# Performance work log

Hardware: AMD Instinct MI355X
Metric: run time of the kernel (lower is better)

The kernel has to match this reference:

```python
import jax, jax.numpy as jnp
import numpy as np

B, N, M = 64, 256, 16
ONF, OEF = 92, 41
NF, EF = 128, 64
FINAL = 128  # final_node_len; final_layer outputs FINAL//2


def _linear_params(key, fan_in, fan_out):
    # kaiming_uniform fan_in, relu: bound = sqrt(6/fan_in)
    bound = np.sqrt(6.0 / fan_in)
    W = jax.random.uniform(key, (fan_out, fan_in), jnp.float32, -bound, bound)
    b = jnp.zeros((fan_out,), jnp.float32)
    return W, b


def setup_inputs() -> dict:
    key = jax.random.key(0)
    ks = jax.random.split(key, 12)
    node_fea = jax.random.normal(ks[0], (B, N, ONF), jnp.float32)
    edge_fea = jax.random.normal(ks[1], (B, N, M, OEF), jnp.float32)
    edge_fea_idx = jax.random.randint(ks[2], (B, N, M), 0, N)
    dis = jax.random.uniform(ks[3], (N, N), jnp.float32)
    Wn, bn = _linear_params(ks[4], ONF, NF)
    We, be = _linear_params(ks[5], OEF, EF)
    W1, b1 = _linear_params(ks[6], 2 * NF + EF, 2 * NF)
    W2, b2 = _linear_params(ks[7], 2 * NF + EF, 2 * NF)
    W3, b3 = _linear_params(ks[8], 2 * NF + EF, 2 * NF)
    Wf, bf = _linear_params(ks[9], NF, FINAL // 2)
    return dict(node_fea=node_fea, edge_fea=edge_fea, edge_fea_idx=edge_fea_idx,
                dis=dis, Wn=Wn, bn=bn, We=We, be=be,
                W1=W1, b1=b1, a1=jnp.float32(0.7),
                W2=W2, b2=b2, a2=jnp.float32(0.7),
                W3=W3, b3=b3, a3=jnp.float32(0.7),
                Wf=Wf, bf=bf,
                DAw=jnp.float32(48.0 / 5.0), DAb=jnp.float32(-28.0 / 5.0))


def _conv(nf, ef, idx, W, b, alpha):
    # nf: [B,N,F]; ef: [B,N,M,E]; idx: [B,N,M]
    Bb, Nn, Mm = idx.shape
    F = nf.shape[-1]
    idx_c = jnp.maximum(idx, 0)
    gathered = jax.vmap(lambda x, i: x[i])(nf, idx_c)           # [B,N,M,F]
    self_exp = jnp.broadcast_to(nf[:, :, None, :], (Bb, Nn, Mm, F))
    total = jnp.concatenate([self_exp, gathered, ef], axis=-1)   # [B,N,M,2F+E]
    gated = jnp.einsum('bnmi,oi->bnmo', total, W) + b            # [B,N,M,2F]
    nbr_filter, nbr_core = jnp.split(gated, 2, axis=-1)
    mask = (idx >= 0).astype(nf.dtype)[..., None]
    nbr_filter = jax.nn.sigmoid(nbr_filter) * mask
    nbr_core = jax.nn.softplus(nbr_core)
    nbr_sumed = jnp.sum(nbr_filter * nbr_core, axis=2)           # [B,N,F]
    return jax.nn.softplus(alpha * nf + nbr_sumed)


def reference(node_fea, edge_fea, edge_fea_idx, dis,
              Wn, bn, We, be,
              W1, b1, a1, W2, b2, a2, W3, b3, a3,
              Wf, bf, DAw, DAb):
    nf = node_fea @ Wn.T + bn                                    # [B,N,NF]
    ef = edge_fea @ We.T + be                                    # [B,N,M,EF]
    nf = _conv(nf, ef, edge_fea_idx, W1, b1, a1)
    nf = _conv(nf, ef, edge_fea_idx, W2, b2, a2)
    nf = _conv(nf, ef, edge_fea_idx, W3, b3, a3)
    nf = nf @ Wf.T + bf                                          # [B,N,FINAL//2]
    DA = jax.nn.sigmoid(DAw * dis + DAb)                         # [N,N]
    node1 = jnp.einsum('ij,bjf->bif', DA, nf)
    return jnp.concatenate([nf, node1], axis=2)                  # [B,N,FINAL]
```

## Files before the change

kernel.cpp:

```cpp
#include <hip/hip_runtime.h>
#include <hip/hip_bf16.h>
#include <math.h>

#define Bb   64
#define Nn   256
#define Mm   16
#define ONF  92
#define OEF  41
#define NF   128
#define EF   64
#define KDIM 320
#define ODIM 256
#define FINAL 128
#define K0C  6
#define NGRP  (Bb * Nn / 4)
#define GRIDP 768

#define LOG2E_F 1.44269504088896f
#define LN2_F   0.6931471805599453f

typedef __attribute__((ext_vector_type(8))) short short8;
typedef __attribute__((ext_vector_type(4))) float f32x4;

#define AS1 __attribute__((address_space(1)))
#define AS3 __attribute__((address_space(3)))

__device__ __forceinline__ void gl2lds16(const void* gp, void* lp) {
    __builtin_amdgcn_global_load_lds((AS1 void*)(void*)gp, (AS3 void*)lp, 16, 0, 0);
}
#define KEEP8(x) asm volatile("" : "+v"(x))

__device__ __forceinline__ float sigmoidf_(float x) {
    float e = __expf(-x);
    return __builtin_amdgcn_rcpf(1.0f + e);
}
__device__ __forceinline__ float softplusf_(float x) {
    return fmaxf(x, 0.0f) + __logf(1.0f + __expf(-fabsf(x)));
}
__device__ __forceinline__ __hip_bfloat16 to_bf16(float x) { return __float2bfloat16(x); }

__device__ __forceinline__ void swz(const float* __restrict__ in, __hip_bfloat16* __restrict__ out,
                                    int t, int Itot, int koff, int Kuse, int K0, float scale)
{
    int j = t & 7;
    int u = t >> 3;
    int lane = u & 63;
    int ln16 = lane & 15, q = lane >> 4;
    int v = u >> 6;
    int k0 = v % K0, tile = v / K0;
    int n = tile * 16 + ln16, k = k0 * 32 + q * 8 + j;
    out[t] = (k < Kuse) ? to_bf16(scale * in[(size_t)n * Itot + koff + k]) : to_bf16(0.0f);
}

#define SZ_WET (OEF * EF)
#define SZ_WB  (16 * K0C * 512)
#define SZ_WS  (16 * 4 * 512)
#define SZ_WNB ((NF / 16) * 3 * 512)
#define SZ_WEB ((EF / 16) * 2 * 512)
#define SZ_WFB ((64 / 16) * 4 * 512)
#define SZ_DA  (Nn * Nn)
#define PREP_TOTAL (SZ_WET + 3 * SZ_WB + 3 * SZ_WS + SZ_WNB + SZ_WEB + SZ_WFB + SZ_DA)

__global__ __launch_bounds__(256) void k_prep(
    const float* __restrict__ We, const float* __restrict__ W1,
    const float* __restrict__ W2, const float* __restrict__ W3,
    const float* __restrict__ Wn, const float* __restrict__ Wf,
    const float* __restrict__ dis, const float* __restrict__ pw, const float* __restrict__ pb,
    float* __restrict__ WeT,
    __hip_bfloat16* __restrict__ W1b, __hip_bfloat16* __restrict__ W2b, __hip_bfloat16* __restrict__ W3b,
    __hip_bfloat16* __restrict__ W1s, __hip_bfloat16* __restrict__ W2s, __hip_bfloat16* __restrict__ W3s,
    __hip_bfloat16* __restrict__ Wnb, __hip_bfloat16* __restrict__ Web, __hip_bfloat16* __restrict__ Wfb,
    __hip_bfloat16* __restrict__ DAf)
{
    int t = blockIdx.x * 256 + threadIdx.x;
    if (t < SZ_WET) {
        int o = t / OEF, i = t - o * OEF;
        WeT[i * EF + o] = We[t];
        return;
    }
    t -= SZ_WET;
    if (t < SZ_WB) { swz(W1, W1b, t, KDIM, NF, 192, K0C, LOG2E_F); return; }
    t -= SZ_WB;
    if (t < SZ_WB) { swz(W2, W2b, t, KDIM, NF, 192, K0C, LOG2E_F); return; }
    t -= SZ_WB;
    if (t < SZ_WB) { swz(W3, W3b, t, KDIM, NF, 192, K0C, LOG2E_F); return; }
    t -= SZ_WB;
    if (t < SZ_WS) { swz(W1, W1s, t, KDIM, 0, NF, 4, LOG2E_F); return; }
    t -= SZ_WS;
    if (t < SZ_WS) { swz(W2, W2s, t, KDIM, 0, NF, 4, LOG2E_F); return; }
    t -= SZ_WS;
    if (t < SZ_WS) { swz(W3, W3s, t, KDIM, 0, NF, 4, LOG2E_F); return; }
    t -= SZ_WS;
    if (t < SZ_WNB) { swz(Wn, Wnb, t, ONF, 0, ONF, 3, 1.0f); return; }
    t -= SZ_WNB;
    if (t < SZ_WEB) { swz(We, Web, t, OEF, 0, OEF, 2, 1.0f); return; }
    t -= SZ_WEB;
    if (t < SZ_WFB) { swz(Wf, Wfb, t, NF, 0, NF, 4, 1.0f); return; }
    t -= SZ_WFB;
    if (t < SZ_DA) {
        int i = t >> 8, jx = t & 255;
        float v = sigmoidf_(fmaf(*pw, dis[t], *pb));
        int itile = i >> 4, ln16 = i & 15;
        int k0 = jx >> 5, q = (jx >> 3) & 3, jj = jx & 7;
        DAf[(size_t)((((itile * 8 + k0) << 6) + (q << 4) + ln16)) * 8 + jj] = to_bf16(v);
    }
}

template<int KIN, int K0, int NCOLS>
__device__ __forceinline__ void emb_body(
    int bid, const float* __restrict__ X, const __hip_bfloat16* __restrict__ Bswz,
    const float* __restrict__ bias, __hip_bfloat16* __restrict__ Y,
    __hip_bfloat16* A_s, __hip_bfloat16* O_s)
{
    constexpr int KP = K0 * 32;
    constexpr int TPW = NCOLS / 64;
    constexpr int OLD = NCOLS + 24;

    const int row0 = bid * 64;
    const int t = threadIdx.x;

    {
        const float4* Xb = (const float4*)(X + (size_t)row0 * KIN);
        constexpr int NV = (64 * KIN) / 4;
        for (int c = t; c < NV; c += 256) {
            float4 v = Xb[c];
            int flat = c * 4;
            #pragma unroll
            for (int e = 0; e < 4; e++) {
                int f = flat + e;
                int row = f / KIN, k = f - row * KIN;
                int mt = row >> 4, ln16 = row & 15;
                int k0 = k >> 5, q = (k >> 3) & 3, j = k & 7;
                float vv = (e == 0) ? v.x : (e == 1) ? v.y : (e == 2) ? v.z : v.w;
                A_s[(((mt * K0 + k0) << 6) + (q << 4) + ln16) * 8 + j] = to_bf16(vv);
            }
        }
        constexpr int PAD = KP - KIN;
        for (int c = t; c < 64 * PAD; c += 256) {
            int row = c / PAD, k = KIN + (c - row * PAD);
            int mt = row >> 4, ln16 = row & 15;
            int k0 = k >> 5, q = (k >> 3) & 3, j = k & 7;
            A_s[(((mt * K0 + k0) << 6) + (q << 4) + ln16) * 8 + j] = to_bf16(0.0f);
        }
    }
    __syncthreads();

    const int wv = t >> 6, lane = t & 63;
    const int q = lane >> 4, ln16 = lane & 15;

    f32x4 acc[4][TPW];
    #pragma unroll
    for (int p = 0; p < TPW; p++) {
        float bv = bias[(wv * TPW + p) * 16 + ln16];
        #pragma unroll
        for (int mt = 0; mt < 4; mt++) acc[mt][p] = (f32x4){bv, bv, bv, bv};
    }

    short8 bw[TPW][K0];
    #pragma unroll
    for (int p = 0; p < TPW; p++)
        #pragma unroll
        for (int k0 = 0; k0 < K0; k0++)
            bw[p][k0] = *(const short8*)(Bswz + ((size_t)((wv * TPW + p) * K0 + k0) << 9) + (lane << 3));

    #pragma unroll
    for (int k0 = 0; k0 < K0; k0++) {
        short8 af[4];
        #pragma unroll
        for (int mt = 0; mt < 4; mt++)
            af[mt] = *(const short8*)(A_s + (((mt * K0 + k0) << 6) + lane) * 8);
        #pragma unroll
        for (int mt = 0; mt < 4; mt++)
            #pragma unroll
            for (int p = 0; p < TPW; p++)
                acc[mt][p] = __builtin_amdgcn_mfma_f32_16x16x32_bf16(af[mt], bw[p][k0], acc[mt][p], 0, 0, 0);
    }

    #pragma unroll
    for (int mt = 0; mt < 4; mt++)
        #pragma unroll
        for (int p = 0; p < TPW; p++) {
            int col = (wv * TPW + p) * 16 + ln16;
            #pragma unroll
            for (int r = 0; r < 4; r++)
                O_s[(mt * 16 + q * 4 + r) * OLD + col] = to_bf16(acc[mt][p][r]);
        }
    __syncthreads();
    constexpr int CH = NCOLS / 8;
    for (int c = t; c < 64 * CH; c += 256) {
        int row = c / CH, ch = c - row * CH;
        *(uint4*)(Y + (size_t)(row0 + row) * NCOLS + ch * 8) =
            *(const uint4*)(O_s + row * OLD + ch * 8);
    }
}

__global__ __launch_bounds__(256) void k_embed_all(
    const float* __restrict__ node_fea, const __hip_bfloat16* __restrict__ Wnb,
    const float* __restrict__ bn, __hip_bfloat16* __restrict__ nf0,
    const float* __restrict__ edge_fea, const __hip_bfloat16* __restrict__ Web,
    const float* __restrict__ be, __hip_bfloat16* __restrict__ efb)
{
    __shared__ __align__(16) __hip_bfloat16 A_s[4 * 3 * 512];
    __shared__ __align__(16) __hip_bfloat16 O_s[64 * (NF + 24)];
    if (blockIdx.x < 256)
        emb_body<ONF, 3, NF>(blockIdx.x, node_fea, Wnb, bn, nf0, A_s, O_s);
    else
        emb_body<OEF, 2, EF>(blockIdx.x - 256, edge_fea, Web, be, efb, A_s, O_s);
}

__global__ __launch_bounds__(256) void k_gemm_s(
    const __hip_bfloat16* __restrict__ nf,
    const __hip_bfloat16* __restrict__ Ws,
    const float* __restrict__ bias,
    float* __restrict__ S)
{
    __shared__ __align__(16) __hip_bfloat16 A_s[16 * 512];
    const int row0 = blockIdx.x * 64;
    const int t = threadIdx.x;
    const int wv = t >> 6, lane = t & 63;
    const int q = lane >> 4, ln16 = lane & 15;

    #pragma unroll
    for (int k0 = 0; k0 < 4; k0++)
        gl2lds16(nf + (size_t)(row0 + (wv << 4) + ln16) * NF + k0 * 32 + q * 8,
                 A_s + ((wv * 4 + k0) * 64 + lane) * 8);
    __syncthreads();

    short8 bw[4][4];
    #pragma unroll
    for (int p = 0; p < 4; p++)
        #pragma unroll
        for (int k0 = 0; k0 < 4; k0++)
            bw[p][k0] = *(const short8*)(Ws + ((size_t)((wv * 4 + p) * 4 + k0) << 9) + (lane << 3));

    f32x4 acc[4][4];
    #pragma unroll
    for (int p = 0; p < 4; p++) {
        float bv = bias[(wv * 4 + p) * 16 + ln16] * LOG2E_F;
        #pragma unroll
        for (int mt = 0; mt < 4; mt++) acc[mt][p] = (f32x4){bv, bv, bv, bv};
    }

    #pragma unroll
    for (int k0 = 0; k0 < 4; k0++) {
        short8 af[4];
        #pragma unroll
        for (int mt = 0; mt < 4; mt++)
            af[mt] = *(const short8*)(A_s + ((mt * 4 + k0) * 64 + lane) * 8);
        #pragma unroll
        for (int mt = 0; mt < 4; mt++)
            #pragma unroll
            for (int p = 0; p < 4; p++)
                acc[mt][p] = __builtin_amdgcn_mfma_f32_16x16x32_bf16(af[mt], bw[p][k0], acc[mt][p], 0, 0, 0);
    }

    #pragma unroll
    for (int mt = 0; mt < 4; mt++)
        #pragma unroll
        for (int p = 0; p < 4; p++) {
            int col = (wv * 4 + p) * 16 + ln16;
            #pragma unroll
            for (int r = 0; r < 4; r++)
                S[(size_t)(row0 + mt * 16 + q * 4 + r) * ODIM + col] = acc[mt][p][r];
        }
}

__global__ __launch_bounds__(256, 3) void k_conv_ps(
    const __hip_bfloat16* __restrict__ nf_in,
    const __hip_bfloat16* __restrict__ ef_bf,
    const int*   __restrict__ eidx,
    const __hip_bfloat16* __restrict__ Wb,
    const float* __restrict__ Sbuf,
    const float* __restrict__ palpha,
    __hip_bfloat16* __restrict__ nf_out)
{
    __shared__ __align__(16) __hip_bfloat16 A_s[2][4 * K0C * 512];

    const int t = threadIdx.x;
    const int wv = t >> 6, lane = t & 63;
    const int q = lane >> 4, ln16 = lane & 15;
    const int row = (wv << 4) + ln16;
    const float alpha = *palpha;

    auto stage_group = [&](int gi, __hip_bfloat16* buf) -> unsigned long long {
        const int node0g = gi * 4;
        const int bbase = node0g & ~255;
        int mi = eidx[node0g * Mm + row];
        unsigned long long mb = __ballot(eidx[node0g * Mm + lane] >= 0);
        int j = mi < 0 ? 0 : mi;
        const __hip_bfloat16* gathp = nf_in + (size_t)(bbase + j) * NF + q * 8;
        #pragma unroll
        for (int k0 = 0; k0 < 4; k0++)
            gl2lds16(gathp + k0 * 32, buf + (wv * K0C + k0) * 512 + lane * 8);
        const __hip_bfloat16* efp = ef_bf + (size_t)((node0g << 4) + row) * EF + q * 8;
        #pragma unroll
        for (int k0 = 0; k0 < 2; k0++)
            gl2lds16(efp + k0 * 32, buf + (wv * K0C + 4 + k0) * 512 + lane * 8);
        return mb;
    };

    const __hip_bfloat16* WF0 = Wb + ((size_t)(2 * wv) * (K0C * 512)) + (lane << 3);
    const __hip_bfloat16* WF1 = WF0 + K0C * 512;
    const __hip_bfloat16* WC0 = WF0 + 8 * (K0C * 512);
    const __hip_bfloat16* WC1 = WC0 + K0C * 512;
    short8 mF0[K0C], mF1[K0C], mC0[K0C], mC1[K0C];
    #pragma unroll
    for (int k0 = 0; k0 < K0C; k0++) {
        mF0[k0] = *(const short8*)(WF0 + k0 * 512);
        mF1[k0] = *(const short8*)(WF1 + k0 * 512);
        mC0[k0] = *(const short8*)(WC0 + k0 * 512);
        mC1[k0] = *(const short8*)(WC1 + k0 * 512);
    }

    int g = blockIdx.x;
    unsigned long long mb_pending = stage_group(g, A_s[0]);
    int cur = 0;

    for (; g < NGRP; g += GRIDP) {
        __syncthreads();

        const unsigned long long mb_now = mb_pending;
        if (g + GRIDP < NGRP) mb_pending = stage_group(g + GRIDP, A_s[cur ^ 1]);

        #pragma unroll
        for (int k0 = 0; k0 < K0C; k0++) {
            KEEP8(mF0[k0]); KEEP8(mF1[k0]); KEEP8(mC0[k0]); KEEP8(mC1[k0]);
        }

        const int node0g = g * 4;
        const __hip_bfloat16* Acur = A_s[cur];

        #pragma unroll
        for (int mt = 0; mt < 4; mt++) {
            const int gnode = node0g + mt;
            const float* Srow = Sbuf + (size_t)gnode * ODIM;
            f32x4 accF[2], accC[2];
            float selfv[2];
            #pragma unroll
            for (int p = 0; p < 2; p++) {
                int col = (2 * wv + p) * 16 + ln16;
                float vF = Srow[col];
                float vC = Srow[128 + col];
                accF[p] = (f32x4){vF, vF, vF, vF};
                accC[p] = (f32x4){vC, vC, vC, vC};
                selfv[p] = __bfloat162float(nf_in[(size_t)gnode * NF + col]);
            }
            #pragma unroll
            for (int k0 = 0; k0 < K0C; k0++) {
                short8 af = *(const short8*)(Acur + ((mt * K0C + k0) * 64 + lane) * 8);
                accF[0] = __builtin_amdgcn_mfma_f32_16x16x32_bf16(af, mF0[k0], accF[0], 0, 0, 0);
                accF[1] = __builtin_amdgcn_mfma_f32_16x16x32_bf16(af, mF1[k0], accF[1], 0, 0, 0);
                accC[0] = __builtin_amdgcn_mfma_f32_16x16x32_bf16(af, mC0[k0], accC[0], 0, 0, 0);
                accC[1] = __builtin_amdgcn_mfma_f32_16x16x32_bf16(af, mC1[k0], accC[1], 0, 0, 0);
            }
            unsigned mbits = (unsigned)(mb_now >> (mt * 16 + q * 4)) & 0xFu;
            #pragma unroll
            for (int p = 0; p < 2; p++) {
                float partial = 0.0f;
                #pragma unroll
                for (int r = 0; r < 4; r++) {
                    bool msk = (mbits >> r) & 1u;
                    float f2 = accF[p][r];
                    float c2 = accC[p][r];
                    float sig = __builtin_amdgcn_rcpf(1.0f + __builtin_amdgcn_exp2f(-f2));
                    float sp2 = fmaxf(c2, 0.0f) +
                                __builtin_amdgcn_logf(1.0f + __builtin_amdgcn_exp2f(-fabsf(c2)));
                    partial += msk ? sig * sp2 : 0.0f;
                }
                partial += __shfl_xor(partial, 16);
                partial += __shfl_xor(partial, 32);
                if (q == 0) {
                    int col = (2 * wv + p) * 16 + ln16;
                    nf_out[(size_t)gnode * NF + col] =
                        to_bf16(softplusf_(fmaf(alpha, selfv[p], LN2_F * partial)));
                }
            }
        }
        cur ^= 1;
    }
}

template<bool PRECOMP>
__global__ __launch_bounds__(256, 3) void k_conv_mfma(
    const __hip_bfloat16* __restrict__ nf_in,
    const float* __restrict__ edge_fea,
    const __hip_bfloat16* __restrict__ ef_bf,
    const int*   __restrict__ eidx,
    const float* __restrict__ WeT,
    const float* __restrict__ be,
    const __hip_bfloat16* __restrict__ Wb,
    const __hip_bfloat16* __restrict__ Wsb,
    const float* __restrict__ bias,
    const float* __restrict__ palpha,
    __hip_bfloat16* __restrict__ nf_out)
{
    __shared__ __align__(16) __hip_bfloat16 A_s[4 * K0C * 512];
    __shared__ __align__(16) __hip_bfloat16 A_sf[4 * 512];

    const int node0 = blockIdx.x * 4;
    const int b = node0 >> 8;
    const int t = threadIdx.x;
    const int wv = t >> 6, lane = t & 63;
    const int q = lane >> 4, ln16 = lane & 15;
    const int row = (wv << 4) + ln16;

    const int myidx = eidx[node0 * Mm + row];
    const unsigned long long mball = __ballot(eidx[node0 * Mm + lane] >= 0);

    float selfv[8];
    #pragma unroll
    for (int mt = 0; mt < 4; mt++)
        #pragma unroll
        for (int p = 0; p < 2; p++)
            selfv[mt * 2 + p] =
                __bfloat162float(nf_in[(size_t)(node0 + mt) * NF + (2 * wv + p) * 16 + ln16]);

    {
        int j = myidx < 0 ? 0 : myidx;
        const __hip_bfloat16* gathp = nf_in + (size_t)((b << 8) + j) * NF;
        #pragma unroll
        for (int k0 = 0; k0 < 4; k0++)
            *(uint4*)(A_s + ((wv * K0C + k0) * 64 + lane) * 8) =
                *(const uint4*)(gathp + k0 * 32 + q * 8);
        *(uint4*)(A_sf + (wv * 64 + lane) * 8) =
            *(const uint4*)(nf_in + (size_t)(node0 + (ln16 & 3)) * NF + wv * 32 + q * 8);
        if (PRECOMP) {
            const __hip_bfloat16* efp = ef_bf + (size_t)((node0 << 4) + row) * EF;
            #pragma unroll
            for (int k0 = 0; k0 < 2; k0++)
                *(uint4*)(A_s + ((wv * K0C + 4 + k0) * 64 + lane) * 8) =
                    *(const uint4*)(efp + k0 * 32 + q * 8);
        } else {
            for (int c = t; c < 64 * EF; c += 256) {
                int rr = c >> 6, col = c & 63;
                float a = be[col];
                const float* er = edge_fea + (size_t)(node0 * Mm + rr) * OEF;
                #pragma unroll
                for (int i = 0; i < OEF; i++) a = fmaf(er[i], WeT[i * EF + col], a);
                int mt = rr >> 4, l16 = rr & 15;
                int k0 = 4 + (col >> 5), qq = (col >> 3) & 3, jj = col & 7;
                A_s[((mt * K0C + k0) * 64 + qq * 16 + l16) * 8 + jj] = to_bf16(a);
            }
        }
    }
    __syncthreads();

    f32x4 sv[4];
    #pragma unroll
    for (int c = 0; c < 4; c++) {
        int tile = 2 * wv + (c & 1) + ((c >> 1) << 3);
        float bv = bias[tile * 16 + ln16] * LOG2E_F;
        sv[c] = (f32x4){bv, bv, bv, bv};
    }
    #pragma unroll
    for (int k0 = 0; k0 < 4; k0++) {
        short8 afs = *(const short8*)(A_sf + (k0 * 64 + lane) * 8);
        #pragma unroll
        for (int c = 0; c < 4; c++) {
            int tile = 2 * wv + (c & 1) + ((c >> 1) << 3);
            short8 bws = *(const short8*)(Wsb + ((size_t)(tile * 4 + k0) << 9) + (lane << 3));
            sv[c] = __builtin_amdgcn_mfma_f32_16x16x32_bf16(afs, bws, sv[c], 0, 0, 0);
        }
    }

    f32x4 accF[4][2], accC[4][2];
    #pragma unroll
    for (int mt = 0; mt < 4; mt++) {
        #pragma unroll
        for (int p = 0; p < 2; p++) {
            float vF = __shfl(sv[p][mt], ln16);
            float vC = __shfl(sv[2 + p][mt], ln16);
            accF[mt][p] = (f32x4){vF, vF, vF, vF};
            accC[mt][p] = (f32x4){vC, vC, vC, vC};
        }
    }

    const __hip_bfloat16* WF0 = Wb + ((size_t)(2 * wv) * (K0C * 512)) + (lane << 3);
    const __hip_bfloat16* WF1 = WF0 + K0C * 512;
    const __hip_bfloat16* WC0 = WF0 + 8 * (K0C * 512);
    const __hip_bfloat16* WC1 = WC0 + K0C * 512;

    #pragma unroll
    for (int k0 = 0; k0 < K0C; k0++) {
        short8 cF0 = *(const short8*)(WF0 + k0 * 512);
        short8 cF1 = *(const short8*)(WF1 + k0 * 512);
        short8 cC0 = *(const short8*)(WC0 + k0 * 512);
        short8 cC1 = *(const short8*)(WC1 + k0 * 512);
        short8 af[4];
        #pragma unroll
        for (int mt = 0; mt < 4; mt++)
            af[mt] = *(const short8*)(A_s + ((mt * K0C + k0) * 64 + lane) * 8);
        #pragma unroll
        for (int mt = 0; mt < 4; mt++) {
            accF[mt][0] = __builtin_amdgcn_mfma_f32_16x16x32_bf16(af[mt], cF0, accF[mt][0], 0, 0, 0);
            accF[mt][1] = __builtin_amdgcn_mfma_f32_16x16x32_bf16(af[mt], cF1, accF[mt][1], 0, 0, 0);
            accC[mt][0] = __builtin_amdgcn_mfma_f32_16x16x32_bf16(af[mt], cC0, accC[mt][0], 0, 0, 0);
            accC[mt][1] = __builtin_amdgcn_mfma_f32_16x16x32_bf16(af[mt], cC1, accC[mt][1], 0, 0, 0);
        }
    }

    const float alpha = *palpha;
    #pragma unroll
    for (int mt = 0; mt < 4; mt++) {
        const int gnode = node0 + mt;
        unsigned mbits = (unsigned)(mball >> (mt * 16 + q * 4)) & 0xFu;
        #pragma unroll
        for (int p = 0; p < 2; p++) {
            float partial = 0.0f;
            #pragma unroll
            for (int r = 0; r < 4; r++) {
                bool msk = (mbits >> r) & 1u;
                float f2 = accF[mt][p][r];
                float c2 = accC[mt][p][r];
                float sig = __builtin_amdgcn_rcpf(1.0f + __builtin_amdgcn_exp2f(-f2));
                float sp2 = fmaxf(c2, 0.0f) +
                            __builtin_amdgcn_logf(1.0f + __builtin_amdgcn_exp2f(-fabsf(c2)));
                partial += msk ? sig * sp2 : 0.0f;
            }
            partial += __shfl_xor(partial, 16);
            partial += __shfl_xor(partial, 32);
            if (q == 0) {
                int col = (2 * wv + p) * 16 + ln16;
                nf_out[(size_t)gnode * NF + col] =
                    to_bf16(softplusf_(fmaf(alpha, selfv[mt * 2 + p], LN2_F * partial)));
            }
        }
    }
}

__global__ __launch_bounds__(256) void k_final_mfma(
    const __hip_bfloat16* __restrict__ nf, const __hip_bfloat16* __restrict__ Wfb,
    const float* __restrict__ bfv, float* __restrict__ out,
    __hip_bfloat16* __restrict__ XT)
{
    __shared__ __align__(16) __hip_bfloat16 A_s[16 * 512];
    const int node0 = blockIdx.x * 64;
    const int bloc = node0 >> 8;
    const int t = threadIdx.x;
    const int wv = t >> 6, lane = t & 63;
    const int q = lane >> 4, ln16 = lane & 15;

    const __hip_bfloat16* rowp = nf + (size_t)(node0 + (wv << 4) + ln16) * NF;
    #pragma unroll
    for (int k0 = 0; k0 < 4; k0++)
        *(uint4*)(A_s + ((wv * 4 + k0) * 64 + lane) * 8) =
            *(const uint4*)(rowp + k0 * 32 + q * 8);
    __syncthreads();

    short8 bw[4];
    #pragma unroll
    for (int k0 = 0; k0 < 4; k0++)
        bw[k0] = *(const short8*)(Wfb + ((size_t)(wv * 4 + k0) * 64 + lane) * 8);

    float bv = bfv[wv * 16 + ln16];
    f32x4 acc[4];
    #pragma unroll
    for (int mt = 0; mt < 4; mt++) acc[mt] = (f32x4){bv, bv, bv, bv};

    #pragma unroll
    for (int k0 = 0; k0 < 4; k0++) {
        short8 af[4];
        #pragma unroll
        for (int mt = 0; mt < 4; mt++)
            af[mt] = *(const short8*)(A_s + ((mt * 4 + k0) * 64 + lane) * 8);
        #pragma unroll
        for (int mt = 0; mt < 4; mt++)
            acc[mt] = __builtin_amdgcn_mfma_f32_16x16x32_bf16(af[mt], bw[k0], acc[mt], 0, 0, 0);
    }

    const int col = (wv << 4) + ln16;
    #pragma unroll
    for (int mt = 0; mt < 4; mt++)
        #pragma unroll
        for (int r = 0; r < 4; r++) {
            int row = mt * 16 + q * 4 + r;
            float v = acc[mt][r];
            out[(size_t)(node0 + row) * FINAL + col] = v;
            XT[(size_t)(bloc * 64 + col) * 256 + (node0 & 255) + row] = to_bf16(v);
        }
}

__global__ __launch_bounds__(256) void k_node1_mfma(
    const __hip_bfloat16* __restrict__ DAf,
    const __hip_bfloat16* __restrict__ XT,
    float* __restrict__ out)
{
    __shared__ __align__(16) __hip_bfloat16 B_s[32 * 512];
    const int blk = blockIdx.x;
    const int b = blk >> 2, i0 = (blk & 3) * 64;
    const int t = threadIdx.x;
    const int wv = t >> 6, lane = t & 63;
    const int q = lane >> 4, ln16 = lane & 15;

    const __hip_bfloat16* xrow = XT + (size_t)(b * 64 + (wv << 4) + ln16) * 256;
    #pragma unroll
    for (int k0 = 0; k0 < 8; k0++)
        *(uint4*)(B_s + ((wv * 8 + k0) * 64 + lane) * 8) =
            *(const uint4*)(xrow + k0 * 32 + q * 8);
    __syncthreads();

    f32x4 acc[4];
    #pragma unroll
    for (int mt = 0; mt < 4; mt++) acc[mt] = (f32x4){0.f, 0.f, 0.f, 0.f};

    #pragma unroll
    for (int k0 = 0; k0 < 8; k0++) {
        short8 bfr = *(const short8*)(B_s + ((wv * 8 + k0) * 64 + lane) * 8);
        short8 af[4];
        #pragma unroll
        for (int mt = 0; mt < 4; mt++)
            af[mt] = *(const short8*)(DAf + (size_t)(((i0 >> 4) + mt) * 8 + k0) * 512 + (lane << 3));
        #pragma unroll
        for (int mt = 0; mt < 4; mt++)
            acc[mt] = __builtin_amdgcn_mfma_f32_16x16x32_bf16(af[mt], bfr, acc[mt], 0, 0, 0);
    }

    #pragma unroll
    for (int mt = 0; mt < 4; mt++)
        #pragma unroll
        for (int r = 0; r < 4; r++) {
            int i = i0 + mt * 16 + q * 4 + r;
            out[(size_t)((b << 8) + i) * FINAL + 64 + (wv << 4) + ln16] = acc[mt][r];
        }
}

extern "C" void kernel_launch(void* const* d_in, const int* in_sizes, int n_in,
                              void* d_out, int out_size, void* d_ws, size_t ws_size,
                              hipStream_t stream)
{
    const float* node_fea = (const float*)d_in[0];
    const float* edge_fea = (const float*)d_in[1];
    const int*   eidx     = (const int*)  d_in[2];
    const float* dis      = (const float*)d_in[3];
    const float* Wn = (const float*)d_in[4];
    const float* bn = (const float*)d_in[5];
    const float* We = (const float*)d_in[6];
    const float* be = (const float*)d_in[7];
    const float* W1 = (const float*)d_in[8];
    const float* b1 = (const float*)d_in[9];
    const float* a1 = (const float*)d_in[10];
    const float* W2 = (const float*)d_in[11];
    const float* b2 = (const float*)d_in[12];
    const float* a2 = (const float*)d_in[13];
    const float* W3 = (const float*)d_in[14];
    const float* b3 = (const float*)d_in[15];
    const float* a3 = (const float*)d_in[16];
    const float* Wf = (const float*)d_in[17];
    const float* bf = (const float*)d_in[18];
    const float* DAw = (const float*)d_in[19];
    const float* DAb = (const float*)d_in[20];
    float* out = (float*)d_out;

    char* base = (char*)d_ws;
    size_t off = 0;
    auto alloc = [&](size_t bytes) { char* p = base + off; off = (off + bytes + 255) & ~(size_t)255; return p; };
    __hip_bfloat16* nfA = (__hip_bfloat16*)alloc((size_t)Bb * Nn * NF * 2);
    __hip_bfloat16* nfB = (__hip_bfloat16*)alloc((size_t)Bb * Nn * NF * 2);
    __hip_bfloat16* W1b = (__hip_bfloat16*)alloc((size_t)SZ_WB * 2);
    __hip_bfloat16* W2b = (__hip_bfloat16*)alloc((size_t)SZ_WB * 2);
    __hip_bfloat16* W3b = (__hip_bfloat16*)alloc((size_t)SZ_WB * 2);
    __hip_bfloat16* W1s = (__hip_bfloat16*)alloc((size_t)SZ_WS * 2);
    __hip_bfloat16* W2s = (__hip_bfloat16*)alloc((size_t)SZ_WS * 2);
    __hip_bfloat16* W3s = (__hip_bfloat16*)alloc((size_t)SZ_WS * 2);
    float* WeT = (float*)alloc((size_t)OEF * EF * 4);
    __hip_bfloat16* DAf = (__hip_bfloat16*)alloc((size_t)Nn * Nn * 2);
    __hip_bfloat16* Wnb = (__hip_bfloat16*)alloc((size_t)SZ_WNB * 2);
    __hip_bfloat16* Web = (__hip_bfloat16*)alloc((size_t)SZ_WEB * 2);
    __hip_bfloat16* Wfb = (__hip_bfloat16*)alloc((size_t)SZ_WFB * 2);
    __hip_bfloat16* XT  = (__hip_bfloat16*)alloc((size_t)Bb * 64 * Nn * 2);
    __hip_bfloat16* efb = (__hip_bfloat16*)alloc((size_t)Bb * Nn * Mm * EF * 2);
    float* Sbuf = (float*)alloc((size_t)Bb * Nn * ODIM * 4);
    const bool precomp = (ws_size >= off);

    hipLaunchKernelGGL(k_prep, dim3((PREP_TOTAL + 255) / 256), dim3(256), 0, stream,
                       We, W1, W2, W3, Wn, Wf, dis, DAw, DAb,
                       WeT, W1b, W2b, W3b, W1s, W2s, W3s, Wnb, Web, Wfb, DAf);

    hipLaunchKernelGGL(k_embed_all, dim3(precomp ? (256 + Bb * Nn * Mm / 64) : 256), dim3(256), 0, stream,
                       node_fea, Wnb, bn, nfA, edge_fea, Web, be, efb);

    if (precomp) {
        hipLaunchKernelGGL(k_gemm_s, dim3(Bb * Nn / 64), dim3(256), 0, stream,
                           nfA, W1s, b1, Sbuf);
        hipLaunchKernelGGL(k_conv_ps, dim3(GRIDP), dim3(256), 0, stream,
                           nfA, efb, eidx, W1b, Sbuf, a1, nfB);
        hipLaunchKernelGGL(k_gemm_s, dim3(Bb * Nn / 64), dim3(256), 0, stream,
                           nfB, W2s, b2, Sbuf);
        hipLaunchKernelGGL(k_conv_ps, dim3(GRIDP), dim3(256), 0, stream,
                           nfB, efb, eidx, W2b, Sbuf, a2, nfA);
        hipLaunchKernelGGL(k_gemm_s, dim3(Bb * Nn / 64), dim3(256), 0, stream,
                           nfA, W3s, b3, Sbuf);
        hipLaunchKernelGGL(k_conv_ps, dim3(GRIDP), dim3(256), 0, stream,
                           nfA, efb, eidx, W3b, Sbuf, a3, nfB);
    } else {
        hipLaunchKernelGGL((k_conv_mfma<false>), dim3(Bb * Nn / 4), dim3(256), 0, stream,
                           nfA, edge_fea, efb, eidx, WeT, be, W1b, W1s, b1, a1, nfB);
        hipLaunchKernelGGL((k_conv_mfma<false>), dim3(Bb * Nn / 4), dim3(256), 0, stream,
                           nfB, edge_fea, efb, eidx, WeT, be, W2b, W2s, b2, a2, nfA);
        hipLaunchKernelGGL((k_conv_mfma<false>), dim3(Bb * Nn / 4), dim3(256), 0, stream,
                           nfA, edge_fea, efb, eidx, WeT, be, W3b, W3s, b3, a3, nfB);
    }

    hipLaunchKernelGGL(k_final_mfma, dim3(Bb * Nn / 64), dim3(256), 0, stream, nfB, Wfb, bf, out, XT);
    hipLaunchKernelGGL(k_node1_mfma, dim3(Bb * 4), dim3(256), 0, stream, DAf, XT, out);
}
```

Before: 313.1 us.

## Restructure conv kernel: weights in LDS, per-wave node groups, A operand in registers

The persistent conv kernel, which kept the weights in registers and double-buffered gathered rows through LDS, is replaced. In the new version each 512-thread block stages half of the output columns' weights in LDS, and each wave loads its gathered neighbor and edge rows straight into registers. Work is split two ways across blocks by output-column half, so every gathered row is loaded twice, but register pressure drops and occupancy can rise. There is no prefetch pipelining now, so the gather latency has to be hidden by having more waves resident.

Result: faster. 300.0 us (-4.2%).

```diff
diff --git a/kernel.cpp b/kernel.cpp
--- a/kernel.cpp
+++ b/kernel.cpp
@@ -13,8 +13,6 @@
 #define ODIM 256
 #define FINAL 128
 #define K0C  6
-#define NGRP  (Bb * Nn / 4)
-#define GRIDP 768
 
 #define LOG2E_F 1.44269504088896f
 #define LN2_F   0.6931471805599453f
@@ -28,7 +26,6 @@
 __device__ __forceinline__ void gl2lds16(const void* gp, void* lp) {
     __builtin_amdgcn_global_load_lds((AS1 void*)(void*)gp, (AS3 void*)lp, 16, 0, 0);
 }
-#define KEEP8(x) asm volatile("" : "+v"(x))
 
 __device__ __forceinline__ float sigmoidf_(float x) {
     float e = __expf(-x);
@@ -265,7 +262,7 @@
         }
 }
 
-__global__ __launch_bounds__(256, 3) void k_conv_ps(
+__global__ __launch_bounds__(512, 4) void k_conv_w(
     const __hip_bfloat16* __restrict__ nf_in,
     const __hip_bfloat16* __restrict__ ef_bf,
     const int*   __restrict__ eidx,
@@ -274,109 +271,110 @@
     const float* __restrict__ palpha,
     __hip_bfloat16* __restrict__ nf_out)
 {
-    __shared__ __align__(16) __hip_bfloat16 A_s[2][4 * K0C * 512];
+    __shared__ __align__(16) __hip_bfloat16 Wl[8 * K0C * 512];
 
     const int t = threadIdx.x;
     const int wv = t >> 6, lane = t & 63;
     const int q = lane >> 4, ln16 = lane & 15;
-    const int row = (wv << 4) + ln16;
+    const int cs = blockIdx.x >> 8;
+    const int gblk = blockIdx.x & 255;
     const float alpha = *palpha;
 
-    auto stage_group = [&](int gi, __hip_bfloat16* buf) -> unsigned long long {
-        const int node0g = gi * 4;
+    #pragma unroll
+    for (int p = 0; p < 6; p++) {
+        int idx = p * 512 + t;
+        int tll = idx / 384;
+        int cin = idx - tll * 384;
+        int gt  = (tll < 4) ? (cs * 4 + tll) : (8 + cs * 4 + (tll - 4));
+        gl2lds16(Wb + (size_t)gt * (K0C * 512) + cin * 8, Wl + (size_t)idx * 8);
+    }
+    __syncthreads();
+
+    #pragma unroll 1
+    for (int task = 0; task < 2; task++) {
+        const int g = gblk * 16 + (task << 3) + wv;
+        const int node0g = g * 4;
         const int bbase = node0g & ~255;
-        int mi = eidx[node0g * Mm + row];
-        unsigned long long mb = __ballot(eidx[node0g * Mm + lane] >= 0);
-        int j = mi < 0 ? 0 : mi;
-        const __hip_bfloat16* gathp = nf_in + (size_t)(bbase + j) * NF + q * 8;
-        #pragma unroll
-        for (int k0 = 0; k0 < 4; k0++)
-            gl2lds16(gathp + k0 * 32, buf + (wv * K0C + k0) * 512 + lane * 8);
-        const __hip_bfloat16* efp = ef_bf + (size_t)((node0g << 4) + row) * EF + q * 8;
-        #pragma unroll
-        for (int k0 = 0; k0 < 2; k0++)
-            gl2lds16(efp + k0 * 32, buf + (wv * K0C + 4 + k0) * 512 + lane * 8);
-        return mb;
-    };
-
-    const __hip_bfloat16* WF0 = Wb + ((size_t)(2 * wv) * (K0C * 512)) + (lane << 3);
-    const __hip_bfloat16* WF1 = WF0 + K0C * 512;
-    const __hip_bfloat16* WC0 = WF0 + 8 * (K0C * 512);
-    const __hip_bfloat16* WC1 = WC0 + K0C * 512;
-    short8 mF0[K0C], mF1[K0C], mC0[K0C], mC1[K0C];
-    #pragma unroll
-    for (int k0 = 0; k0 < K0C; k0++) {
-        mF0[k0] = *(const short8*)(WF0 + k0 * 512);
-        mF1[k0] = *(const short8*)(WF1 + k0 * 512);
-        mC0[k0] = *(const short8*)(WC0 + k0 * 512);
-        mC1[k0] = *(const short8*)(WC1 + k0 * 512);
-    }
-
-    int g = blockIdx.x;
-    unsigned long long mb_pending = stage_group(g, A_s[0]);
-    int cur = 0;
-
-    for (; g < NGRP; g += GRIDP) {
-        __syncthreads();
-
-        const unsigned long long mb_now = mb_pending;
-        if (g + GRIDP < NGRP) mb_pending = stage_group(g + GRIDP, A_s[cur ^ 1]);
-
-        #pragma unroll
-        for (int k0 = 0; k0 < K0C; k0++) {
-            KEEP8(mF0[k0]); KEEP8(mF1[k0]); KEEP8(mC0[k0]); KEEP8(mC1[k0]);
-        }
-
-        const int node0g = g * 4;
-        const __hip_bfloat16* Acur = A_s[cur];
-
-        #pragma unroll
-        for (int mt = 0; mt < 4; mt++) {
-            const int gnode = node0g + mt;
-            const float* Srow = Sbuf + (size_t)gnode * ODIM;
-            f32x4 accF[2], accC[2];
-            float selfv[2];
-            #pragma unroll
-            for (int p = 0; p < 2; p++) {
-                int col = (2 * wv + p) * 16 + ln16;
-                float vF = Srow[col];
-                float vC = Srow[128 + col];
-                accF[p] = (f32x4){vF, vF, vF, vF};
-                accC[p] = (f32x4){vC, vC, vC, vC};
-                selfv[p] = __bfloat162float(nf_in[(size_t)gnode * NF + col]);
+        const int jv = eidx[(node0g << 4) + lane];
+        const unsigned long long mball = __ballot(jv >= 0);
+
+        #pragma unroll 1
+        for (int h = 0; h < 2; h++) {
+            short8 afr[2][K0C];
+            #pragma unroll
+            for (int mtl = 0; mtl < 2; mtl++) {
+                const int mt = 2 * h + mtl;
+                int jm = __shfl(jv, (mt << 4) + ln16);
+                jm = jm < 0 ? 0 : jm;
+                const __hip_bfloat16* gp = nf_in + (size_t)(bbase + jm) * NF + q * 8;
+                #pragma unroll
+                for (int k0 = 0; k0 < 4; k0++)
+                    afr[mtl][k0] = *(const short8*)(gp + k0 * 32);
+                const __hip_bfloat16* ep =
+                    ef_bf + ((size_t)((node0g + mt) << 4) + ln16) * EF + q * 8;
+                afr[mtl][4] = *(const short8*)(ep);
+                afr[mtl][5] = *(const short8*)(ep + 32);
             }
-            #pragma unroll
-            for (int k0 = 0; k0 < K0C; k0++) {
-                short8 af = *(const short8*)(Acur + ((mt * K0C + k0) * 64 + lane) * 8);
-                accF[0] = __builtin_amdgcn_mfma_f32_16x16x32_bf16(af, mF0[k0], accF[0], 0, 0, 0);
-                accF[1] = __builtin_amdgcn_mfma_f32_16x16x32_bf16(af, mF1[k0], accF[1], 0, 0, 0);
-                accC[0] = __builtin_amdgcn_mfma_f32_16x16x32_bf16(af, mC0[k0], accC[0], 0, 0, 0);
-                accC[1] = __builtin_amdgcn_mfma_f32_16x16x32_bf16(af, mC1[k0], accC[1], 0, 0, 0);
-            }
-            unsigned mbits = (unsigned)(mb_now >> (mt * 16 + q * 4)) & 0xFu;
-            #pragma unroll
-            for (int p = 0; p < 2; p++) {
-                float partial = 0.0f;
+
+            float sF[2][4], sC[2][4], svv[2][4];
+            #pragma unroll
+            for (int mtl = 0; mtl < 2; mtl++) {
+                const int gnode = node0g + 2 * h + mtl;
+                const float* Sr = Sbuf + (size_t)gnode * ODIM + cs * 64 + ln16;
+                const __hip_bfloat16* nr = nf_in + (size_t)gnode * NF + cs * 64 + ln16;
                 #pragma unroll
-                for (int r = 0; r < 4; r++) {
-                    bool msk = (mbits >> r) & 1u;
-                    float f2 = accF[p][r];
-                    float c2 = accC[p][r];
-                    float sig = __builtin_amdgcn_rcpf(1.0f + __builtin_amdgcn_exp2f(-f2));
-                    float sp2 = fmaxf(c2, 0.0f) +
-                                __builtin_amdgcn_logf(1.0f + __builtin_amdgcn_exp2f(-fabsf(c2)));
-                    partial += msk ? sig * sp2 : 0.0f;
-                }
-                partial += __shfl_xor(partial, 16);
-                partial += __shfl_xor(partial, 32);
-                if (q == 0) {
-                    int col = (2 * wv + p) * 16 + ln16;
-                    nf_out[(size_t)gnode * NF + col] =
-                        to_bf16(softplusf_(fmaf(alpha, selfv[p], LN2_F * partial)));
+                for (int c = 0; c < 4; c++) {
+                    sF[mtl][c] = Sr[c * 16];
+                    sC[mtl][c] = Sr[128 + c * 16];
+                    svv[mtl][c] = __bfloat162float(nr[c * 16]);
                 }
             }
-        }
-        cur ^= 1;
+
+            #pragma unroll 1
+            for (int ctl = 0; ctl < 4; ctl++) {
+                f32x4 accF[2], accC[2];
+                #pragma unroll
+                for (int mtl = 0; mtl < 2; mtl++) {
+                    float vF = sF[mtl][ctl], vC = sC[mtl][ctl];
+                    accF[mtl] = (f32x4){vF, vF, vF, vF};
+                    accC[mtl] = (f32x4){vC, vC, vC, vC};
+                }
+                #pragma unroll
+                for (int k0 = 0; k0 < K0C; k0++) {
+                    short8 wF = *(const short8*)(Wl + (((ctl)     * K0C + k0) << 9) + (lane << 3));
+                    short8 wC = *(const short8*)(Wl + (((4 + ctl) * K0C + k0) << 9) + (lane << 3));
+                    #pragma unroll
+                    for (int mtl = 0; mtl < 2; mtl++) {
+                        accF[mtl] = __builtin_amdgcn_mfma_f32_16x16x32_bf16(afr[mtl][k0], wF, accF[mtl], 0, 0, 0);
+                        accC[mtl] = __builtin_amdgcn_mfma_f32_16x16x32_bf16(afr[mtl][k0], wC, accC[mtl], 0, 0, 0);
+                    }
+                }
+                #pragma unroll
+                for (int mtl = 0; mtl < 2; mtl++) {
+                    const int mt = 2 * h + mtl;
+                    const int gnode = node0g + mt;
+                    unsigned mbits = (unsigned)(mball >> ((mt << 4) + (q << 2))) & 0xFu;
+                    float partial = 0.0f;
+                    #pragma unroll
+                    for (int r = 0; r < 4; r++) {
+                        bool msk = (mbits >> r) & 1u;
+                        float f2 = accF[mtl][r];
+                        float c2 = accC[mtl][r];
+                        float sig = __builtin_amdgcn_rcpf(1.0f + __builtin_amdgcn_exp2f(-f2));
+                        float sp2 = fmaxf(c2, 0.0f) +
+                                    __builtin_amdgcn_logf(1.0f + __builtin_amdgcn_exp2f(-fabsf(c2)));
+                        partial += msk ? sig * sp2 : 0.0f;
+                    }
+                    partial += __shfl_xor(partial, 16);
+                    partial += __shfl_xor(partial, 32);
+                    if (q == 0) {
+                        int col = cs * 64 + ctl * 16 + ln16;
+                        nf_out[(size_t)gnode * NF + col] =
+                            to_bf16(softplusf_(fmaf(alpha, svv[mtl][ctl], LN2_F * partial)));
+                    }
+                }
+            }
+        }
     }
 }
 
@@ -682,15 +680,15 @@
     if (precomp) {
         hipLaunchKernelGGL(k_gemm_s, dim3(Bb * Nn / 64), dim3(256), 0, stream,
                            nfA, W1s, b1, Sbuf);
-        hipLaunchKernelGGL(k_conv_ps, dim3(GRIDP), dim3(256), 0, stream,
+        hipLaunchKernelGGL(k_conv_w, dim3(512), dim3(512), 0, stream,
                            nfA, efb, eidx, W1b, Sbuf, a1, nfB);
         hipLaunchKernelGGL(k_gemm_s, dim3(Bb * Nn / 64), dim3(256), 0, stream,
                            nfB, W2s, b2, Sbuf);
-        hipLaunchKernelGGL(k_conv_ps, dim3(GRIDP), dim3(256), 0, stream,
+        hipLaunchKernelGGL(k_conv_w, dim3(512), dim3(512), 0, stream,
                            nfB, efb, eidx, W2b, Sbuf, a2, nfA);
         hipLaunchKernelGGL(k_gemm_s, dim3(Bb * Nn / 64), dim3(256), 0, stream,
                            nfA, W3s, b3, Sbuf);
-        hipLaunchKernelGGL(k_conv_ps, dim3(GRIDP), dim3(256), 0, stream,
+        hipLaunchKernelGGL(k_conv_w, dim3(512), dim3(512), 0, stream,
                            nfA, efb, eidx, W3b, Sbuf, a3, nfB);
     } else {
         hipLaunchKernelGGL((k_conv_mfma<false>), dim3(Bb * Nn / 4), dim3(256), 0, stream,
```
